# Performance work log

Measured on AMD Instinct MI355X. Metric: run time of the kernel, lower is better.

Reference implementation:

```python
import jax, jax.numpy as jnp
import numpy as np

N, C, D = 1024, 151, 4096   # num boxes, num classes (VG-150+bg), hidden_dim*8
NMS_THRESH = 0.5            # cfg.TEST.RELATION.LATER_NMS_PREDICTION_THRES


def setup_inputs() -> dict:
    key = jax.random.key(0)
    k1, k2, k3, k4 = jax.random.split(key, 4)
    obj_fmap = jax.random.normal(k1, (N, D), jnp.float32)
    W_out = jax.random.normal(k2, (D, C), jnp.float32) / np.sqrt(D).astype(np.float32)
    b_out = jnp.zeros((C,), jnp.float32)
    # valid xyxy boxes: top-left in [0,800), width/height in [16,208)
    xy = jax.random.uniform(k3, (N, C, 2), jnp.float32, 0.0, 800.0)
    wh = jax.random.uniform(k4, (N, C, 2), jnp.float32, 16.0, 208.0)
    boxes_per_cls = jnp.concatenate([xy, xy + wh], axis=-1)  # [N, C, 4]
    return {"obj_fmap": obj_fmap, "W_out": W_out, "b_out": b_out,
            "boxes_per_cls": boxes_per_cls}


def nms_overlaps(boxes):
    """Per-class pairwise IoU. boxes: [N, C, 4] xyxy -> [N, N, C].
    Matches neural-motifs nms_overlaps (uses the +1 pixel convention)."""
    max_xy = jnp.minimum(boxes[:, None, :, 2:], boxes[None, :, :, 2:])  # [N,N,C,2]
    min_xy = jnp.maximum(boxes[:, None, :, :2], boxes[None, :, :, :2])  # [N,N,C,2]
    inter_wh = jnp.clip(max_xy - min_xy + 1.0, 0.0)
    inters = inter_wh[..., 0] * inter_wh[..., 1]                         # [N,N,C]
    areas = (boxes[..., 2] - boxes[..., 0] + 1.0) * \
            (boxes[..., 3] - boxes[..., 1] + 1.0)                        # [N,C]
    union = areas[None, :, :] + areas[:, None, :] - inters
    return inters / union


def greedy_commit(probs, is_overlap):
    """Greedy per-box class commitment with overlap suppression.
    probs: [N,C] (background col already zeroed); is_overlap: [N,N,C] bool."""
    n, c = probs.shape
    row_ids = jnp.arange(n)
    col_ids = jnp.arange(c)

    def body(i, state):
        p, commits = state
        flat = jnp.argmax(p)
        b, cl = flat // c, flat % c
        commits = jnp.where(row_ids == b, cl, commits)
        ov = is_overlap[b, :, cl]                      # [N] dynamic gather
        # zero column cl for overlapping boxes
        p = jnp.where((col_ids[None, :] == cl) & ov[:, None], 0.0, p)
        # retire the committed box
        p = jnp.where((row_ids == b)[:, None], -1.0, p)
        return p, commits

    _, commits = jax.lax.fori_loop(0, n, body,
                                   (probs, jnp.zeros((n,), jnp.int32)))
    return commits


def reference(obj_fmap, W_out, b_out, boxes_per_cls):
    # decoder: obj_dists2 = self.out_obj(obj_fmap)
    obj_dists = obj_fmap @ W_out + b_out                 # [N, C]
    # sgdet eval branch: softmax scores, zero background, greedy NMS commit
    probs = jax.nn.softmax(obj_dists, axis=-1)
    probs = probs.at[:, 0].set(0.0)
    is_overlap = nms_overlaps(boxes_per_cls) >= NMS_THRESH  # [N,N,C] bool
    obj_preds = greedy_commit(probs, is_overlap)            # [N] int32
    return obj_dists, obj_preds
```

## Files before the change

kernel.cpp:

```cpp
#include <hip/hip_runtime.h>

#define NB 1024
#define NC 151
#define NCP 152
#define DF 4096
typedef unsigned long long u64;

__global__ __launch_bounds__(384) void gemm_sm_kernel(
    const float* __restrict__ fmap, const float* __restrict__ W,
    const float* __restrict__ bias, float* __restrict__ dists,
    float* __restrict__ probs) {
  __shared__ float sf[4 * DF];
  __shared__ double spart[2][4][NC];
  __shared__ float sdist[4][NCP];
  __shared__ float smx[4], ssum[4];
  int r0 = blockIdx.x * 4;
  const float4* src = (const float4*)(fmap + (size_t)r0 * DF);
  for (int i = threadIdx.x; i < 4 * (DF / 4); i += 384) {
    int r = i >> 10;
    int q = i & 1023;
    float4 v = src[i];
    sf[(4 * q + 0) * 4 + r] = v.x;
    sf[(4 * q + 1) * 4 + r] = v.y;
    sf[(4 * q + 2) * 4 + r] = v.z;
    sf[(4 * q + 3) * 4 + r] = v.w;
  }
  __syncthreads();
  {
    int half = (threadIdx.x >= 192) ? 1 : 0;
    int ch = threadIdx.x - half * 192;
    if (ch < NC) {
      double a0 = 0.0, a1 = 0.0, a2 = 0.0, a3 = 0.0;
      const float4* sf4 = (const float4*)sf + half * (DF / 2);
      const float* w = W + ch + (size_t)half * (DF / 2) * NC;
#pragma unroll 8
      for (int d = 0; d < DF / 2; ++d) {
        float4 f = sf4[d];
        double wv = (double)w[(size_t)d * NC];
        a0 += (double)f.x * wv;
        a1 += (double)f.y * wv;
        a2 += (double)f.z * wv;
        a3 += (double)f.w * wv;
      }
      spart[half][0][ch] = a0;
      spart[half][1][ch] = a1;
      spart[half][2][ch] = a2;
      spart[half][3][ch] = a3;
    }
  }
  __syncthreads();
  int c = threadIdx.x;
  if (c < NC) {
    float b = bias[c];
    float v0 = (float)(spart[0][0][c] + spart[1][0][c]) + b;
    float v1 = (float)(spart[0][1][c] + spart[1][1][c]) + b;
    float v2 = (float)(spart[0][2][c] + spart[1][2][c]) + b;
    float v3 = (float)(spart[0][3][c] + spart[1][3][c]) + b;
    dists[(size_t)(r0 + 0) * NC + c] = v0;
    dists[(size_t)(r0 + 1) * NC + c] = v1;
    dists[(size_t)(r0 + 2) * NC + c] = v2;
    dists[(size_t)(r0 + 3) * NC + c] = v3;
    sdist[0][c] = v0; sdist[1][c] = v1; sdist[2][c] = v2; sdist[3][c] = v3;
  }
  __syncthreads();
  if (threadIdx.x < 64) {
    int t = threadIdx.x;
#pragma unroll
    for (int r = 0; r < 4; ++r) {
      float v0 = sdist[r][t];
      float v1 = sdist[r][t + 64];
      float v2 = (t + 128 < NC) ? sdist[r][t + 128] : -3.0e38f;
      float m = fmaxf(fmaxf(v0, v1), v2);
      for (int off = 32; off; off >>= 1) m = fmaxf(m, __shfl_down(m, off));
      m = __shfl(m, 0);
      float e0 = expf(v0 - m), e1 = expf(v1 - m);
      float e2 = (t + 128 < NC) ? expf(v2 - m) : 0.0f;
      float s = e0 + e1 + e2;
      for (int off = 32; off; off >>= 1) s += __shfl_down(s, off);
      s = __shfl(s, 0);
      if (t == 0) { smx[r] = m; ssum[r] = s; }
    }
  }
  __syncthreads();
  if (c < NC) {
#pragma unroll
    for (int r = 0; r < 4; ++r) {
      float p = (c == 0) ? 0.0f : (expf(sdist[r][c] - smx[r]) / ssum[r]);
      probs[(size_t)(r0 + r) * NCP + c] = p;
    }
  }
  if (threadIdx.x == 0) {
#pragma unroll
    for (int r = 0; r < 4; ++r) probs[(size_t)(r0 + r) * NCP + NC] = -1.0f;
  }
}

__global__ __launch_bounds__(256) void mask_kernel(
    const float* __restrict__ boxes, u64* __restrict__ mask) {
#pragma clang fp contract(off)
  int cl = blockIdx.x >> 4;
  int bb = (blockIdx.x & 15) * 64;
  __shared__ float4 sbox[NB];
  __shared__ float sarea[NB];
  for (int i = threadIdx.x; i < NB; i += 256) {
    float4 b = *(const float4*)(boxes + ((size_t)i * NC + cl) * 4);
    sbox[i] = b;
    sarea[i] = (b.z - b.x + 1.0f) * (b.w - b.y + 1.0f);
  }
  __syncthreads();
  int wv = threadIdx.x >> 6, lane = threadIdx.x & 63;
  for (int j = 0; j < 16; ++j) {
    int b = bb + wv * 16 + j;
    float4 B = sbox[b];
    float areaB = sarea[b];
    u64 myword = 0;
#pragma unroll
    for (int k = 0; k < 16; ++k) {
      int r = k * 64 + lane;
      float4 R = sbox[r];
      float ix = fminf(B.z, R.z) - fmaxf(B.x, R.x) + 1.0f;
      float iy = fminf(B.w, R.w) - fmaxf(B.y, R.y) + 1.0f;
      ix = fmaxf(ix, 0.0f);
      iy = fmaxf(iy, 0.0f);
      float inter = ix * iy;
      float uni = sarea[r] + areaB - inter;
      float iou = inter / uni;
      u64 bal = __ballot(iou >= 0.5f);
      if (lane == k) myword = bal;
    }
    if (lane < 16) mask[((size_t)cl * NB + b) * 16 + lane] = myword;
  }
}

template <int CTRL, int ROWMASK>
__device__ __forceinline__ float dpp_max_step(float v) {
  int x = __float_as_int(v);
  int t = __builtin_amdgcn_update_dpp(x, x, CTRL, ROWMASK, 0xf, false);
  return fmaxf(v, __int_as_float(t));
}

__device__ __forceinline__ float wave_max(float v) {
  v = dpp_max_step<0x111, 0xf>(v);
  v = dpp_max_step<0x112, 0xf>(v);
  v = dpp_max_step<0x114, 0xf>(v);
  v = dpp_max_step<0x118, 0xf>(v);
  v = dpp_max_step<0x142, 0xa>(v);
  v = dpp_max_step<0x143, 0xc>(v);
  return __int_as_float(__builtin_amdgcn_readlane(__float_as_int(v), 63));
}

__device__ __forceinline__ void rescan_row(const float* __restrict__ pp,
                                           u64 z0, u64 z1, u64 z2,
                                           float& mo, int& ao) {
  const float4* p4 = (const float4*)pp;
  float m = 0.0f; int a = 0;
#pragma unroll 2
  for (int q = 0; q < NCP / 4; ++q) {
    float4 v = p4[q];
    u64 z = q < 16 ? z0 : (q < 32 ? z1 : z2);
    unsigned bits = (unsigned)(z >> ((q & 15) * 4)) & 0xFu;
    int c0 = q * 4;
    float vx = (bits & 1u) ? 0.0f : v.x;
    float vy = (bits & 2u) ? 0.0f : v.y;
    float vz = (bits & 4u) ? 0.0f : v.z;
    float vw = (bits & 8u) ? 0.0f : v.w;
    if (vx > m) { m = vx; a = c0; }
    if (vy > m) { m = vy; a = c0 + 1; }
    if (vz > m) { m = vz; a = c0 + 2; }
    if (vw > m) { m = vw; a = c0 + 3; }
  }
  mo = m; ao = a;
}

__global__ __launch_bounds__(256, 1) void greedy_kernel(
    const float* __restrict__ probs, const u64* __restrict__ mask,
    float* __restrict__ out_preds) {
  __shared__ u64 smask[NB * 16];
  __shared__ unsigned pcls[NB];
  __shared__ u64 skey[2][4];

  int tid = threadIdx.x;
  int w = tid >> 6, lane = tid & 63;
  int rbase = tid << 2;
  int widx = tid >> 4;
  int hsh = (tid & 15) << 2;

  float rm[4];
  int ra[4], cm[4];
  u64 zb0[4], zb1[4], zb2[4];
  unsigned committed = 0;

#pragma unroll
  for (int r = 0; r < 4; ++r) {
    rescan_row(probs + (size_t)(rbase + r) * NCP, 0, 0, 0, rm[r], ra[r]);
    cm[r] = 0; zb0[r] = 0; zb1[r] = 0; zb2[r] = 0;
    pcls[rbase + r] = (unsigned)ra[r];
  }
  __syncthreads();

  for (int j = 0; j < NB; j += 16) {
    int col = j + (tid >> 4);
    int wd = tid & 15;
    unsigned pc = pcls[col];
    smask[(col << 4) | wd] = mask[(((size_t)pc << 10) | (size_t)col) * 16 + wd];
  }
  __syncthreads();

  for (int it = 0; it < NB; ++it) {
    int par = it & 1;

    float bv = rm[0];
    int bp = ra[0];
#pragma unroll
    for (int r = 1; r < 4; ++r) {
      int p = (r << 8) | ra[r];
      bool t = rm[r] > bv;
      bv = t ? rm[r] : bv;
      bp = t ? p : bp;
    }

    float wmax = wave_max(bv);
    u64 ball = __ballot(bv == wmax);
    int wl = __ffsll(ball) - 1;
    int pw = __builtin_amdgcn_readlane(bp, wl);
    int gw = (w << 8) | (wl << 2) | (pw >> 8);
    int clw = pw & 0xff;
    unsigned ub = __float_as_uint(wmax);
    unsigned su = ((int)ub >= 0) ? (ub | 0x80000000u) : ~ub;
    u64 key = ((u64)su << 32) | ((u64)(NB - 1 - gw) << 8) | (unsigned)clw;
    if (lane == 0) skey[par][w] = key;
    __syncthreads();

    u64 k0 = skey[par][0], k1 = skey[par][1], k2 = skey[par][2], k3 = skey[par][3];
    u64 ka = k0 > k1 ? k0 : k1;
    u64 kb = k2 > k3 ? k2 : k3;
    u64 kk = ka > kb ? ka : kb;
    int b = NB - 1 - (int)((kk >> 8) & 0x3FFu);
    int cl = (int)(kk & 0xFFu);
    if ((unsigned)(kk >> 32) < 0x80000000u) cl = 0;

    u64 word = smask[(b << 4) | widx];
    unsigned pc = pcls[b];
    if ((unsigned)cl != pc) {
      word = mask[(((size_t)cl << 10) | (size_t)b) * 16 + widx];
    }
    unsigned hits = (unsigned)(word >> hsh) & 0xFu;

    int wi = cl >> 6;
    u64 bmv = 1ull << (cl & 63);
    u64 m0 = (wi == 0) ? bmv : 0, m1 = (wi == 1) ? bmv : 0, m2 = (wi == 2) ? bmv : 0;

    bool meT = (tid == (b >> 2));
    int blo = b & 3;

    unsigned need = 0;
#pragma unroll
    for (int r = 0; r < 4; ++r) {
      unsigned rb = 1u << r;
      bool hit = (hits & rb) != 0;
      if (r == blo) {
        if (meT) { committed |= rb; rm[r] = -1.0f; cm[r] = cl; hit = false; }
      }
      if (hit) {
        if (committed & rb) {
          if (rm[r] < 0.0f) { rm[r] = 0.0f; ra[r] = cl; }
          else if (cl < ra[r]) ra[r] = cl;
        } else {
          zb0[r] |= m0; zb1[r] |= m1; zb2[r] |= m2;
          if (ra[r] == cl) need |= rb;
        }
      }
    }
    if (__ballot(need != 0)) {
#pragma unroll
      for (int r = 0; r < 4; ++r) {
        if (need & (1u << r))
          rescan_row(probs + (size_t)(rbase + r) * NCP,
                     zb0[r], zb1[r], zb2[r], rm[r], ra[r]);
      }
    }
  }

#pragma unroll
  for (int r = 0; r < 4; ++r)
    out_preds[rbase + r] = (float)cm[r];
}

extern "C" void kernel_launch(void* const* d_in, const int* in_sizes, int n_in,
                              void* d_out, int out_size, void* d_ws, size_t ws_size,
                              hipStream_t stream) {
  const float* obj_fmap = (const float*)d_in[0];
  const float* W_out    = (const float*)d_in[1];
  const float* b_out    = (const float*)d_in[2];
  const float* boxes    = (const float*)d_in[3];

  float* out_dists = (float*)d_out;
  float* out_preds = (float*)d_out + NB * NC;

  float* probs = (float*)d_ws;
  u64*   mask  = (u64*)(probs + (size_t)NB * NCP);

  gemm_sm_kernel<<<NB / 4, 384, 0, stream>>>(obj_fmap, W_out, b_out, out_dists, probs);
  mask_kernel<<<NC * 16, 256, 0, stream>>>(boxes, mask);
  greedy_kernel<<<1, 256, 0, stream>>>(probs, mask, out_preds);
}
```

Baseline: 1.002 ms.

## Cache second-best class per row in greedy loop and split GEMM K four ways

The greedy kernel now tracks the top two classes per row. When the best class of a row is suppressed, the cached runner-up is promoted and no rescan of the probability row is needed; a full rescan happens only once both are gone. Separately, the GEMM kernel doubles its block to 768 threads and splits the K dimension into four partial sums, adding parallelism at the cost of more registers and shared memory per block. Together these aim to shorten the serial greedy loop and the GEMM. The extra comparisons add register pressure in the single-block greedy kernel.

```diff
diff --git a/kernel.cpp b/kernel.cpp
--- a/kernel.cpp
+++ b/kernel.cpp
@@ -6,17 +6,17 @@
 #define DF 4096
 typedef unsigned long long u64;
 
-__global__ __launch_bounds__(384) void gemm_sm_kernel(
+__global__ __launch_bounds__(768) void gemm_sm_kernel(
     const float* __restrict__ fmap, const float* __restrict__ W,
     const float* __restrict__ bias, float* __restrict__ dists,
     float* __restrict__ probs) {
   __shared__ float sf[4 * DF];
-  __shared__ double spart[2][4][NC];
+  __shared__ double spart[4][4][NC];
   __shared__ float sdist[4][NCP];
   __shared__ float smx[4], ssum[4];
   int r0 = blockIdx.x * 4;
   const float4* src = (const float4*)(fmap + (size_t)r0 * DF);
-  for (int i = threadIdx.x; i < 4 * (DF / 4); i += 384) {
+  for (int i = threadIdx.x; i < 4 * (DF / 4); i += 768) {
     int r = i >> 10;
     int q = i & 1023;
     float4 v = src[i];
@@ -27,14 +27,14 @@
   }
   __syncthreads();
   {
-    int half = (threadIdx.x >= 192) ? 1 : 0;
-    int ch = threadIdx.x - half * 192;
+    int qr = threadIdx.x / 192;
+    int ch = threadIdx.x - qr * 192;
     if (ch < NC) {
       double a0 = 0.0, a1 = 0.0, a2 = 0.0, a3 = 0.0;
-      const float4* sf4 = (const float4*)sf + half * (DF / 2);
-      const float* w = W + ch + (size_t)half * (DF / 2) * NC;
+      const float4* sf4 = (const float4*)sf + qr * (DF / 4);
+      const float* w = W + ch + (size_t)qr * (DF / 4) * NC;
 #pragma unroll 8
-      for (int d = 0; d < DF / 2; ++d) {
+      for (int d = 0; d < DF / 4; ++d) {
         float4 f = sf4[d];
         double wv = (double)w[(size_t)d * NC];
         a0 += (double)f.x * wv;
@@ -42,20 +42,20 @@
         a2 += (double)f.z * wv;
         a3 += (double)f.w * wv;
       }
-      spart[half][0][ch] = a0;
-      spart[half][1][ch] = a1;
-      spart[half][2][ch] = a2;
-      spart[half][3][ch] = a3;
+      spart[qr][0][ch] = a0;
+      spart[qr][1][ch] = a1;
+      spart[qr][2][ch] = a2;
+      spart[qr][3][ch] = a3;
     }
   }
   __syncthreads();
   int c = threadIdx.x;
   if (c < NC) {
     float b = bias[c];
-    float v0 = (float)(spart[0][0][c] + spart[1][0][c]) + b;
-    float v1 = (float)(spart[0][1][c] + spart[1][1][c]) + b;
-    float v2 = (float)(spart[0][2][c] + spart[1][2][c]) + b;
-    float v3 = (float)(spart[0][3][c] + spart[1][3][c]) + b;
+    float v0 = (float)(((spart[0][0][c] + spart[1][0][c]) + spart[2][0][c]) + spart[3][0][c]) + b;
+    float v1 = (float)(((spart[0][1][c] + spart[1][1][c]) + spart[2][1][c]) + spart[3][1][c]) + b;
+    float v2 = (float)(((spart[0][2][c] + spart[1][2][c]) + spart[2][2][c]) + spart[3][2][c]) + b;
+    float v3 = (float)(((spart[0][3][c] + spart[1][3][c]) + spart[2][3][c]) + spart[3][3][c]) + b;
     dists[(size_t)(r0 + 0) * NC + c] = v0;
     dists[(size_t)(r0 + 1) * NC + c] = v1;
     dists[(size_t)(r0 + 2) * NC + c] = v2;
@@ -149,27 +149,32 @@
   return __int_as_float(__builtin_amdgcn_readlane(__float_as_int(v), 63));
 }
 
-__device__ __forceinline__ void rescan_row(const float* __restrict__ pp,
-                                           u64 z0, u64 z1, u64 z2,
-                                           float& mo, int& ao) {
+template <bool MASKED>
+__device__ __forceinline__ void scan_top2(const float* __restrict__ pp,
+                                          u64 z0, u64 z1, u64 z2,
+                                          float& m1o, int& a1o, float& m2o, int& a2o) {
   const float4* p4 = (const float4*)pp;
-  float m = 0.0f; int a = 0;
+  float m1 = -1.0f, m2 = -1.0f;
+  int a1 = 0, a2 = 0;
 #pragma unroll 2
   for (int q = 0; q < NCP / 4; ++q) {
     float4 v = p4[q];
-    u64 z = q < 16 ? z0 : (q < 32 ? z1 : z2);
-    unsigned bits = (unsigned)(z >> ((q & 15) * 4)) & 0xFu;
+    unsigned bits = 0;
+    if (MASKED) {
+      u64 z = q < 16 ? z0 : (q < 32 ? z1 : z2);
+      bits = (unsigned)(z >> ((q & 15) * 4)) & 0xFu;
+    }
+    float e0 = (MASKED && (bits & 1u)) ? 0.0f : v.x;
+    float e1 = (MASKED && (bits & 2u)) ? 0.0f : v.y;
+    float e2 = (MASKED && (bits & 4u)) ? 0.0f : v.z;
+    float e3 = (MASKED && (bits & 8u)) ? 0.0f : v.w;
     int c0 = q * 4;
-    float vx = (bits & 1u) ? 0.0f : v.x;
-    float vy = (bits & 2u) ? 0.0f : v.y;
-    float vz = (bits & 4u) ? 0.0f : v.z;
-    float vw = (bits & 8u) ? 0.0f : v.w;
-    if (vx > m) { m = vx; a = c0; }
-    if (vy > m) { m = vy; a = c0 + 1; }
-    if (vz > m) { m = vz; a = c0 + 2; }
-    if (vw > m) { m = vw; a = c0 + 3; }
-  }
-  mo = m; ao = a;
+    if (e0 > m1) { m2 = m1; a2 = a1; m1 = e0; a1 = c0; } else if (e0 > m2) { m2 = e0; a2 = c0; }
+    if (e1 > m1) { m2 = m1; a2 = a1; m1 = e1; a1 = c0 + 1; } else if (e1 > m2) { m2 = e1; a2 = c0 + 1; }
+    if (e2 > m1) { m2 = m1; a2 = a1; m1 = e2; a1 = c0 + 2; } else if (e2 > m2) { m2 = e2; a2 = c0 + 2; }
+    if (e3 > m1) { m2 = m1; a2 = a1; m1 = e3; a1 = c0 + 3; } else if (e3 > m2) { m2 = e3; a2 = c0 + 3; }
+  }
+  m1o = m1; a1o = a1; m2o = m2; a2o = a2;
 }
 
 __global__ __launch_bounds__(256, 1) void greedy_kernel(
@@ -185,14 +190,15 @@
   int widx = tid >> 4;
   int hsh = (tid & 15) << 2;
 
-  float rm[4];
-  int ra[4], cm[4];
+  float rm[4], rm2[4];
+  int ra[4], ra2[4], cm[4];
   u64 zb0[4], zb1[4], zb2[4];
   unsigned committed = 0;
 
 #pragma unroll
   for (int r = 0; r < 4; ++r) {
-    rescan_row(probs + (size_t)(rbase + r) * NCP, 0, 0, 0, rm[r], ra[r]);
+    scan_top2<false>(probs + (size_t)(rbase + r) * NCP, 0, 0, 0,
+                     rm[r], ra[r], rm2[r], ra2[r]);
     cm[r] = 0; zb0[r] = 0; zb1[r] = 0; zb2[r] = 0;
     pcls[rbase + r] = (unsigned)ra[r];
   }
@@ -259,7 +265,9 @@
       unsigned rb = 1u << r;
       bool hit = (hits & rb) != 0;
       if (r == blo) {
-        if (meT) { committed |= rb; rm[r] = -1.0f; cm[r] = cl; hit = false; }
+        if (meT) {
+          committed |= rb; rm[r] = -1.0f; rm2[r] = -3.0f; cm[r] = cl; hit = false;
+        }
       }
       if (hit) {
         if (committed & rb) {
@@ -267,7 +275,14 @@
           else if (cl < ra[r]) ra[r] = cl;
         } else {
           zb0[r] |= m0; zb1[r] |= m1; zb2[r] |= m2;
-          if (ra[r] == cl) need |= rb;
+          if (rm2[r] >= 0.0f && ra2[r] == cl) rm2[r] = -3.0f;
+          if (ra[r] == cl) {
+            if (rm2[r] >= 0.0f) {
+              rm[r] = rm2[r]; ra[r] = ra2[r]; rm2[r] = -3.0f;
+            } else {
+              need |= rb;
+            }
+          }
         }
       }
     }
@@ -275,8 +290,9 @@
 #pragma unroll
       for (int r = 0; r < 4; ++r) {
         if (need & (1u << r))
-          rescan_row(probs + (size_t)(rbase + r) * NCP,
-                     zb0[r], zb1[r], zb2[r], rm[r], ra[r]);
+          scan_top2<true>(probs + (size_t)(rbase + r) * NCP,
+                          zb0[r], zb1[r], zb2[r],
+                          rm[r], ra[r], rm2[r], ra2[r]);
       }
     }
   }
@@ -300,7 +316,7 @@
   float* probs = (float*)d_ws;
   u64*   mask  = (u64*)(probs + (size_t)NB * NCP);
 
-  gemm_sm_kernel<<<NB / 4, 384, 0, stream>>>(obj_fmap, W_out, b_out, out_dists, probs);
+  gemm_sm_kernel<<<NB / 4, 768, 0, stream>>>(obj_fmap, W_out, b_out, out_dists, probs);
   mask_kernel<<<NC * 16, 256, 0, stream>>>(boxes, mask);
   greedy_kernel<<<1, 256, 0, stream>>>(probs, mask, out_preds);
 }
```

Result: no change. 1.006 ms (+0.4%).
